# Performance work log

Measured on AMD Instinct MI355X. Metric: run time of the kernel, lower is better.

Reference implementation:

```python
import jax, jax.numpy as jnp
import numpy as np
from jax import lax

B, P, C = 2, 512, 5                 # images, proposals/img, classes (incl. background)
IN_FEAT, REP = 12544, 1024          # 256*7*7 pooled features; TwoMLPHead width
H_IMG = W_IMG = 800.0
SCORE_THRESH, NMS_THRESH, DET_PER_IMG = 0.05, 0.5, 100
MIN_SIZE = 0.01
WX, WY, WW, WH = 10.0, 10.0, 5.0, 5.0
BBOX_CLIP = float(np.log(1000.0 / 16.0))
NEG = -1e9


def _make_boxes(key, n):
    k1, k2, k3, k4 = jax.random.split(key, 4)
    cx = jax.random.uniform(k1, (n,)) * W_IMG
    cy = jax.random.uniform(k2, (n,)) * H_IMG
    bw = jax.random.uniform(k3, (n,)) * 180.0 + 20.0
    bh = jax.random.uniform(k4, (n,)) * 180.0 + 20.0
    x1 = jnp.clip(cx - bw / 2, 0.0, W_IMG)
    y1 = jnp.clip(cy - bh / 2, 0.0, H_IMG)
    x2 = jnp.clip(cx + bw / 2, 0.0, W_IMG)
    y2 = jnp.clip(cy + bh / 2, 0.0, H_IMG)
    return jnp.stack([x1, y1, x2, y2], -1).astype(jnp.float32)


def setup_inputs() -> dict:
    ks = jax.random.split(jax.random.key(0), 12)
    box_features = jax.random.normal(ks[0], (B * P, IN_FEAT), jnp.float32)
    proposals = jnp.stack([_make_boxes(ks[1 + i], P) for i in range(B)])
    def w(k, shp):
        return (jax.random.normal(k, shp, jnp.float32) / np.sqrt(shp[0])).astype(jnp.float32)
    return {
        'box_features': box_features,
        'proposals': proposals,
        'W1': w(ks[3], (IN_FEAT, REP)), 'b1': jnp.zeros((REP,), jnp.float32),
        'W2': w(ks[4], (REP, REP)),     'b2': jnp.zeros((REP,), jnp.float32),
        'Wc': w(ks[5], (REP, C)),       'bc': jnp.zeros((C,), jnp.float32),
        'Wb': w(ks[6], (REP, 4 * C)),   'bb': jnp.zeros((4 * C,), jnp.float32),
    }


def box_iou(a, b):
    area_a = (a[:, 2] - a[:, 0]) * (a[:, 3] - a[:, 1])
    area_b = (b[:, 2] - b[:, 0]) * (b[:, 3] - b[:, 1])
    lt = jnp.maximum(a[:, None, :2], b[None, :, :2])
    rb = jnp.minimum(a[:, None, 2:], b[None, :, 2:])
    wh = jnp.clip(rb - lt, 0.0)
    inter = wh[..., 0] * wh[..., 1]
    return inter / (area_a[:, None] + area_b[None, :] - inter + 1e-9)


def decode(reg, props):
    # reg: [N, C, 4] raw deltas; props: [N, 4] xyxy  (torchvision BoxCoder.decode)
    w = props[:, 2] - props[:, 0]
    h = props[:, 3] - props[:, 1]
    cx = props[:, 0] + 0.5 * w
    cy = props[:, 1] + 0.5 * h
    dx, dy = reg[..., 0] / WX, reg[..., 1] / WY
    dw = jnp.minimum(reg[..., 2] / WW, BBOX_CLIP)
    dh = jnp.minimum(reg[..., 3] / WH, BBOX_CLIP)
    pcx = dx * w[:, None] + cx[:, None]
    pcy = dy * h[:, None] + cy[:, None]
    pw = jnp.exp(dw) * w[:, None]
    ph = jnp.exp(dh) * h[:, None]
    return jnp.stack([pcx - 0.5 * pw, pcy - 0.5 * ph, pcx + 0.5 * pw, pcy + 0.5 * ph], -1)


def postprocess_one(boxes, scores, labels):
    # boxes [M,4] (already clipped), scores [M], labels [M] int; fixed-size output.
    M = boxes.shape[0]
    ws = boxes[:, 2] - boxes[:, 0]
    hs = boxes[:, 3] - boxes[:, 1]
    valid = (scores > SCORE_THRESH) & (ws >= MIN_SIZE) & (hs >= MIN_SIZE)
    order = jnp.argsort(-scores)
    b, s, l, v = boxes[order], scores[order], labels[order], valid[order]
    # batched (per-class) NMS via class-offset trick
    off = l.astype(b.dtype)[:, None] * (max(H_IMG, W_IMG) + 1.0)
    iou = box_iou(b + off, b + off)
    idxs = jnp.arange(M)

    def body(i, keep):
        sup = (iou[i] > NMS_THRESH) & keep[i] & (idxs > i)
        return keep & ~sup

    keep = lax.fori_loop(0, M, body, v)
    sc = jnp.where(keep, s, NEG)
    top_s, top_i = lax.top_k(sc, DET_PER_IMG)
    ok = top_s > NEG / 2
    tb = jnp.where(ok[:, None], b[top_i], 0.0)
    tl = jnp.where(ok, l[top_i], 0)
    ts = jnp.where(ok, top_s, 0.0)
    return tb, ts, tl


def reference(box_features, proposals, W1, b1, W2, b2, Wc, bc, Wb, bb):
    # box_head: TwoMLPHead
    h = jax.nn.relu(box_features @ W1 + b1)
    h = jax.nn.relu(h @ W2 + b2)
    # box_predictor
    class_logits = h @ Wc + bc                       # [N, C]
    box_regression = (h @ Wb + bb).reshape(-1, C, 4)  # [N, C, 4]
    props = proposals.reshape(-1, 4)
    pred = decode(box_regression, props)             # [N, C, 4]
    # clip to image
    pred = jnp.stack([
        jnp.clip(pred[..., 0], 0.0, W_IMG), jnp.clip(pred[..., 1], 0.0, H_IMG),
        jnp.clip(pred[..., 2], 0.0, W_IMG), jnp.clip(pred[..., 3], 0.0, H_IMG)], -1)
    scores = jax.nn.softmax(class_logits, -1)        # [N, C]
    # drop background class, flatten proposal-major (matches torch reshape(-1,4))
    pb = pred[:, 1:, :].reshape(B, P * (C - 1), 4)
    sc = scores[:, 1:].reshape(B, P * (C - 1))
    labels = jnp.tile(jnp.arange(1, C, dtype=jnp.int32), P)  # [M]
    boxes_o, scores_o, labels_o = jax.vmap(postprocess_one, in_axes=(0, 0, None))(pb, sc, labels)
    return boxes_o, scores_o, labels_o
```

## Files before the change

kernel.cpp:

```cpp
#include <hip/hip_runtime.h>
#include <math.h>

#define NROWS 1024
#define K1    12544
#define REP   1024
#define NDET  2048
#define DETS  100
#define BBOX_CLIP_F 4.135166556742356f

typedef __attribute__((ext_vector_type(8))) short bf16x8;
typedef __attribute__((ext_vector_type(4))) float f32x4;

__device__ __forceinline__ unsigned short rne_bf16(float x) {
  unsigned u = __float_as_uint(x);
  u += 0x7fffu + ((u >> 16) & 1u);
  return (unsigned short)(u >> 16);
}
__device__ __forceinline__ float bf16f(unsigned short h) {
  return __uint_as_float(((unsigned)h) << 16);
}
__device__ __forceinline__ int swz(int r, int s) {
  return s ^ (r & 3) ^ ((r >> 2) & 3);
}
__device__ __forceinline__ void gload16(const void* g, void* lds) {
  __builtin_amdgcn_global_load_lds(
      (const __attribute__((address_space(1))) unsigned int*)g,
      (__attribute__((address_space(3))) unsigned int*)lds, 16, 0, 0);
}

__global__ __launch_bounds__(256) void pack_b(
    const float* __restrict__ W, unsigned short* __restrict__ Oh,
    unsigned short* __restrict__ Ol, int nKB) {
  __shared__ unsigned short th[32 * 36], tl[32 * 36];
  const int kb = blockIdx.x, n0 = blockIdx.y * 32;
  const int t = threadIdx.x;
  const int r = t >> 3, c4 = (t & 7) << 2;
  float4 v = *(const float4*)&W[(size_t)(kb * 32 + r) * REP + n0 + c4];
  float fv[4] = {v.x, v.y, v.z, v.w};
#pragma unroll
  for (int j = 0; j < 4; ++j) {
    unsigned short h = rne_bf16(fv[j]);
    th[(c4 + j) * 36 + r] = h;
    tl[(c4 + j) * 36 + r] = rne_bf16(fv[j] - bf16f(h));
  }
  __syncthreads();
  const int half = t >> 7;
  const int n_loc = (t & 127) >> 2, slot = t & 3;
  const unsigned short* src = (half ? tl : th) + n_loc * 36 + slot * 8;
  ushort4 u0 = *(const ushort4*)src;
  ushort4 u1 = *(const ushort4*)(src + 4);
  const int n = n0 + n_loc, rb = n >> 7, rr = n & 127;
  size_t chunk = ((size_t)(rb * nKB + kb)) * 512 + rr * 4 + swz(rr, slot);
  unsigned short* dst = (half ? Ol : Oh) + chunk * 8;
  *(ushort4*)dst = u0;
  *(ushort4*)(dst + 4) = u1;
}

__global__ __launch_bounds__(256) void gemm_pk(
    const float* __restrict__ A, const unsigned short* __restrict__ Bh,
    const unsigned short* __restrict__ Bl, float* __restrict__ T,
    int K, int nKB, int stepsPerZ) {
  __shared__ __align__(16) unsigned short lds[2][4][4096];
  const int tid = threadIdx.x;
  const int w = tid >> 6, l = tid & 63;
  const int bm = blockIdx.x * 128;
  const int bnb = blockIdx.y;
  const int tk0 = blockIdx.z * stepsPerZ;
  const int arow = tid >> 1, ahalf = tid & 1;
  const int fr = l & 15, q = l >> 4;
  const int wr = (w >> 1) * 64, wc = (w & 1) * 64;
  const int qs = q ^ (fr & 3) ^ (fr >> 2);
  const int aoff = ((wr + fr) * 4 + qs) * 16;
  const int boff = ((wc + fr) * 4 + qs) * 16;
  const float* aptr = A + (size_t)(bm + arow) * K + ahalf * 16;

  float4 av[4];
  auto loadA = [&](int tk) {
    const float* p = aptr + tk * 32;
#pragma unroll
    for (int j = 0; j < 4; ++j) av[j] = *(const float4*)(p + j * 4);
  };
  auto stageB = [&](int bf, int tk) {
    const unsigned short* gh = Bh + ((size_t)(bnb * nKB + tk)) * 4096;
    const unsigned short* gl_ = Bl + ((size_t)(bnb * nKB + tk)) * 4096;
#pragma unroll
    for (int rseg = 0; rseg < 2; ++rseg) {
      const int seg = rseg * 4 + w;
      gload16(gh + (size_t)(seg * 64 + l) * 8, &lds[bf][2][seg * 512]);
      gload16(gl_ + (size_t)(seg * 64 + l) * 8, &lds[bf][3][seg * 512]);
    }
  };
  auto writeA = [&](int bf) {
#pragma unroll
    for (int j = 0; j < 2; ++j) {
      const int s_ = ahalf * 2 + j;
      float fv[8] = {av[j * 2].x, av[j * 2].y, av[j * 2].z, av[j * 2].w,
                     av[j * 2 + 1].x, av[j * 2 + 1].y, av[j * 2 + 1].z, av[j * 2 + 1].w};
      unsigned hp[4], lp[4];
#pragma unroll
      for (int p2 = 0; p2 < 4; ++p2) {
        unsigned short h0 = rne_bf16(fv[2 * p2]), h1 = rne_bf16(fv[2 * p2 + 1]);
        float l0 = fv[2 * p2] - bf16f(h0), l1 = fv[2 * p2 + 1] - bf16f(h1);
        hp[p2] = (unsigned)h0 | ((unsigned)h1 << 16);
        lp[p2] = (unsigned)rne_bf16(l0) | ((unsigned)rne_bf16(l1) << 16);
      }
      const int chunk = arow * 4 + swz(arow, s_);
      *(uint4*)&lds[bf][0][chunk * 8] = make_uint4(hp[0], hp[1], hp[2], hp[3]);
      *(uint4*)&lds[bf][1][chunk * 8] = make_uint4(lp[0], lp[1], lp[2], lp[3]);
    }
  };

  f32x4 acc[4][4];
#pragma unroll
  for (int m = 0; m < 4; ++m)
#pragma unroll
    for (int n = 0; n < 4; ++n) acc[m][n] = (f32x4){0.f, 0.f, 0.f, 0.f};

  loadA(tk0);
  stageB(0, tk0);
  writeA(0);
  __syncthreads();
  int cur = 0;
  for (int s = 0; s < stepsPerZ; ++s) {
    const bool nx = (s + 1 < stepsPerZ);
    if (nx) { loadA(tk0 + s + 1); stageB(cur ^ 1, tk0 + s + 1); }
    const char* La = (const char*)&lds[cur][0][0];
    const char* Ll = (const char*)&lds[cur][1][0];
    const char* Lbh = (const char*)&lds[cur][2][0];
    const char* Lbl = (const char*)&lds[cur][3][0];
    bf16x8 ah[4], al[4], bh[4], bl[4];
#pragma unroll
    for (int m = 0; m < 4; ++m) {
      ah[m] = *(const bf16x8*)(La + aoff + m * 1024);
      al[m] = *(const bf16x8*)(Ll + aoff + m * 1024);
    }
#pragma unroll
    for (int n = 0; n < 4; ++n) {
      bh[n] = *(const bf16x8*)(Lbh + boff + n * 1024);
      bl[n] = *(const bf16x8*)(Lbl + boff + n * 1024);
    }
#pragma unroll
    for (int m = 0; m < 4; ++m)
#pragma unroll
      for (int n = 0; n < 4; ++n) {
        acc[m][n] = __builtin_amdgcn_mfma_f32_16x16x32_bf16(ah[m], bh[n], acc[m][n], 0, 0, 0);
        acc[m][n] = __builtin_amdgcn_mfma_f32_16x16x32_bf16(ah[m], bl[n], acc[m][n], 0, 0, 0);
        acc[m][n] = __builtin_amdgcn_mfma_f32_16x16x32_bf16(al[m], bh[n], acc[m][n], 0, 0, 0);
      }
    if (nx) writeA(cur ^ 1);
    __syncthreads();
    cur ^= 1;
  }
  float* Tz = T + (size_t)blockIdx.z * (NROWS * REP);
#pragma unroll
  for (int m = 0; m < 4; ++m) {
    const int r0 = bm + wr + m * 16 + ((l >> 4) << 2);
#pragma unroll
    for (int n = 0; n < 4; ++n) {
      const int c = bnb * 128 + wc + n * 16 + fr;
#pragma unroll
      for (int j = 0; j < 4; ++j) Tz[(size_t)(r0 + j) * REP + c] = acc[m][n][j];
    }
  }
}

__global__ __launch_bounds__(256) void combine8_relu(
    const float* __restrict__ T, const float* __restrict__ bias, float* __restrict__ H) {
  const int i = blockIdx.x * 256 + threadIdx.x;
  const int MN4 = NROWS * REP / 4;
  const float4* t = (const float4*)T;
  float4 s0 = t[i];
#pragma unroll
  for (int z = 1; z < 8; ++z) {
    float4 v = t[i + z * MN4];
    s0.x += v.x; s0.y += v.y; s0.z += v.z; s0.w += v.w;
  }
  float4 bs = ((const float4*)bias)[i & 255];
  float4 r;
  r.x = fmaxf(s0.x + bs.x, 0.f);
  r.y = fmaxf(s0.y + bs.y, 0.f);
  r.z = fmaxf(s0.z + bs.z, 0.f);
  r.w = fmaxf(s0.w + bs.w, 0.f);
  ((float4*)H)[i] = r;
}

__global__ __launch_bounds__(256) void gemm64(
    const float* __restrict__ A, const float* __restrict__ W,
    float* __restrict__ T, int K, int N, int kChunk) {
  __shared__ float As[32][68];
  __shared__ float Bs[32][64];
  const int tid = threadIdx.x;
  const int bm = blockIdx.x * 64, bn = blockIdx.y * 64;
  const int k0 = blockIdx.z * kChunk;
  const int tx = tid & 15, ty = tid >> 4;
  const int ar = tid >> 3;
  const int ac = (tid & 7) << 2;
  const int br = tid >> 4;
  const int bc = (tid & 15) << 2;
  float acc[4][4] = {{0.f,0.f,0.f,0.f},{0.f,0.f,0.f,0.f},{0.f,0.f,0.f,0.f},{0.f,0.f,0.f,0.f}};
  for (int kk = k0; kk < k0 + kChunk; kk += 32) {
    float4 a0 = *(const float4*)&A[(size_t)(bm + ar) * K + kk + ac];
    float4 a1 = *(const float4*)&A[(size_t)(bm + ar + 32) * K + kk + ac];
    float4 b0 = *(const float4*)&W[(size_t)(kk + br) * N + bn + bc];
    float4 b1 = *(const float4*)&W[(size_t)(kk + br + 16) * N + bn + bc];
    As[ac+0][ar] = a0.x; As[ac+1][ar] = a0.y; As[ac+2][ar] = a0.z; As[ac+3][ar] = a0.w;
    As[ac+0][ar+32] = a1.x; As[ac+1][ar+32] = a1.y; As[ac+2][ar+32] = a1.z; As[ac+3][ar+32] = a1.w;
    *(float4*)&Bs[br][bc]    = b0;
    *(float4*)&Bs[br+16][bc] = b1;
    __syncthreads();
#pragma unroll
    for (int k = 0; k < 32; ++k) {
      float4 av = *(const float4*)&As[k][ty << 2];
      float4 bv = *(const float4*)&Bs[k][tx << 2];
      float a_[4] = {av.x, av.y, av.z, av.w};
      float b_[4] = {bv.x, bv.y, bv.z, bv.w};
#pragma unroll
      for (int i = 0; i < 4; ++i)
#pragma unroll
        for (int j = 0; j < 4; ++j)
          acc[i][j] = fmaf(a_[i], b_[j], acc[i][j]);
    }
    __syncthreads();
  }
  float* Tz = T + (size_t)blockIdx.z * NROWS * REP;
#pragma unroll
  for (int i = 0; i < 4; ++i) {
    float4 v = make_float4(acc[i][0], acc[i][1], acc[i][2], acc[i][3]);
    *(float4*)&Tz[(size_t)(bm + (ty << 2) + i) * N + bn + (tx << 2)] = v;
  }
}

__global__ __launch_bounds__(256) void combine_relu(
    const float* __restrict__ T, const float* __restrict__ bias, float* __restrict__ H) {
  const int i = blockIdx.x * 256 + threadIdx.x;
  const int MN4 = NROWS * REP / 4;
  const float4* t = (const float4*)T;
  float4 a = t[i], b = t[i + MN4], c = t[i + 2 * MN4], d = t[i + 3 * MN4];
  float4 bs = ((const float4*)bias)[i & 255];
  float4 r;
  r.x = fmaxf(((a.x + b.x) + (c.x + d.x)) + bs.x, 0.f);
  r.y = fmaxf(((a.y + b.y) + (c.y + d.y)) + bs.y, 0.f);
  r.z = fmaxf(((a.z + b.z) + (c.z + d.z)) + bs.z, 0.f);
  r.w = fmaxf(((a.w + b.w) + (c.w + d.w)) + bs.w, 0.f);
  ((float4*)H)[i] = r;
}

__global__ __launch_bounds__(256) void heads_kernel(
    const float* __restrict__ H2, const float* __restrict__ Wc, const float* __restrict__ bcv,
    const float* __restrict__ Wb, const float* __restrict__ bbv,
    const float* __restrict__ props, float* __restrict__ pb, float* __restrict__ sc) {
  const int n = blockIdx.x;
  __shared__ float hrow[REP];
  __shared__ float part[25][8];
  __shared__ float outv[25];
  __shared__ float smax[5];
  const int tid = threadIdx.x;
  ((float4*)hrow)[tid] = ((const float4*)(H2 + (size_t)n * REP))[tid];
  __syncthreads();
  if (tid < 200) {
    const int o = tid >> 3, s = tid & 7;
    float a = 0.f;
    if (o < 5) {
      const float* w = Wc + o;
      for (int k = s * 128; k < s * 128 + 128; ++k) a = fmaf(hrow[k], w[(size_t)k * 5], a);
    } else {
      const float* w = Wb + (o - 5);
      for (int k = s * 128; k < s * 128 + 128; ++k) a = fmaf(hrow[k], w[(size_t)k * 20], a);
    }
    part[o][s] = a;
  }
  __syncthreads();
  if (tid < 25) {
    float a = ((part[tid][0] + part[tid][1]) + (part[tid][2] + part[tid][3]))
            + ((part[tid][4] + part[tid][5]) + (part[tid][6] + part[tid][7]));
    a += (tid < 5) ? bcv[tid] : bbv[tid - 5];
    outv[tid] = a;
  }
  __syncthreads();
  if (tid == 0) {
    float m = outv[0];
    for (int c = 1; c < 5; ++c) m = fmaxf(m, outv[c]);
    float e[5], ssum = 0.f;
    for (int c = 0; c < 5; ++c) { e[c] = expf(outv[c] - m); ssum += e[c]; }
    for (int c = 0; c < 5; ++c) smax[c] = e[c] / ssum;
  }
  __syncthreads();
  if (tid < 4) {
    const int c = tid + 1;
    const float* pr = props + (size_t)n * 4;
    const float x1 = pr[0], y1 = pr[1], x2 = pr[2], y2 = pr[3];
    const float w = x2 - x1, h = y2 - y1;
    const float cx = x1 + 0.5f * w, cy = y1 + 0.5f * h;
    const float r0 = outv[5 + c * 4 + 0], r1 = outv[5 + c * 4 + 1];
    const float r2 = outv[5 + c * 4 + 2], r3 = outv[5 + c * 4 + 3];
    const float dx = r0 / 10.0f, dy = r1 / 10.0f;
    const float dw = fminf(r2 / 5.0f, BBOX_CLIP_F);
    const float dh = fminf(r3 / 5.0f, BBOX_CLIP_F);
    const float pcx = dx * w + cx, pcy = dy * h + cy;
    const float pw = expf(dw) * w, ph = expf(dh) * h;
    float bx1 = pcx - 0.5f * pw, by1 = pcy - 0.5f * ph;
    float bx2 = pcx + 0.5f * pw, by2 = pcy + 0.5f * ph;
    bx1 = fminf(fmaxf(bx1, 0.f), 800.f);
    by1 = fminf(fmaxf(by1, 0.f), 800.f);
    bx2 = fminf(fmaxf(bx2, 0.f), 800.f);
    by2 = fminf(fmaxf(by2, 0.f), 800.f);
    const int img = n >> 9;
    const int pidx = ((n & 511) << 2) + (c - 1);
    float* o = pb + (size_t)(img * NDET + pidx) * 4;
    o[0] = bx1; o[1] = by1; o[2] = bx2; o[3] = by2;
    sc[img * NDET + pidx] = smax[c];
  }
}

__global__ __launch_bounds__(1024) void sort_kernel(
    const float* __restrict__ sc, unsigned* __restrict__ sidx) {
  const int b = blockIdx.x;
  __shared__ unsigned long long key[NDET];
  const int tid = threadIdx.x;
  for (int t = tid; t < NDET; t += 1024) {
    unsigned bits = __float_as_uint(sc[b * NDET + t]);
    key[t] = ((unsigned long long)bits << 32) | (unsigned)(~t);
  }
  __syncthreads();
  for (int k = 2; k <= NDET; k <<= 1) {
    for (int j = k >> 1; j > 0; j >>= 1) {
      for (int t = tid; t < NDET; t += 1024) {
        const int ixj = t ^ j;
        if (ixj > t) {
          const bool up = (t & k) == 0;
          unsigned long long a = key[t], bb_ = key[ixj];
          if ((a < bb_) == up) { key[t] = bb_; key[ixj] = a; }
        }
      }
      __syncthreads();
    }
  }
  for (int t = tid; t < NDET; t += 1024)
    sidx[b * NDET + t] = ~(unsigned)key[t];
}

__global__ __launch_bounds__(256) void prep_kernel(
    const unsigned* __restrict__ sidx, const float* __restrict__ pb, const float* __restrict__ sc,
    float* __restrict__ sbox, float* __restrict__ soff, float* __restrict__ sscore,
    float* __restrict__ sarea, float* __restrict__ slab, unsigned* __restrict__ vword) {
  const int b = blockIdx.y;
  const int i = blockIdx.x * 256 + threadIdx.x;
  const unsigned oi = sidx[b * NDET + i];
  const float* bx = pb + (size_t)(b * NDET + oi) * 4;
  const float x1 = bx[0], y1 = bx[1], x2 = bx[2], y2 = bx[3];
  const float s = sc[b * NDET + oi];
  const float lab = (float)((oi & 3) + 1);
  const bool valid = (s > 0.05f) && ((x2 - x1) >= 0.01f) && ((y2 - y1) >= 0.01f);
  const float off = lab * 801.0f;
  float* sb = sbox + (size_t)(b * NDET + i) * 4;
  sb[0] = x1; sb[1] = y1; sb[2] = x2; sb[3] = y2;
  float* so = soff + (size_t)(b * NDET + i) * 4;
  so[0] = x1 + off; so[1] = y1 + off; so[2] = x2 + off; so[3] = y2 + off;
  sscore[b * NDET + i] = s;
  sarea[b * NDET + i] = (x2 - x1) * (y2 - y1);
  slab[b * NDET + i] = lab;
  const unsigned long long bal = __ballot(valid);
  if ((i & 31) == 0) vword[b * 64 + (i >> 5)] = (unsigned)(bal >> (i & 32));
}

__global__ __launch_bounds__(256) void mask_kernel(
    const float* __restrict__ soff, const float* __restrict__ sarea,
    unsigned* __restrict__ mask) {
  const int b = blockIdx.y;
  __shared__ float box[NDET][4];
  __shared__ float area[NDET];
  const int tid = threadIdx.x;
  const float4* src = (const float4*)(soff + (size_t)b * NDET * 4);
  for (int t = tid; t < NDET; t += 256) ((float4*)box)[t] = src[t];
  const float4* asrc = (const float4*)(sarea + (size_t)b * NDET);
  for (int t = tid; t < NDET / 4; t += 256) ((float4*)area)[t] = asrc[t];
  __syncthreads();
  const int li = tid >> 6;
  const int w  = tid & 63;
  const int i  = blockIdx.x * 4 + li;
  const float ax1 = box[i][0], ay1 = box[i][1], ax2 = box[i][2], ay2 = box[i][3];
  const float aa = area[i];
  unsigned bits = 0;
#pragma unroll 4
  for (int jj = 0; jj < 32; ++jj) {
    const int j = jj * 64 + w;
    const float ix = fmaxf(fminf(ax2, box[j][2]) - fmaxf(ax1, box[j][0]), 0.f);
    const float iy = fmaxf(fminf(ay2, box[j][3]) - fmaxf(ay1, box[j][1]), 0.f);
    const float inter = ix * iy;
    const float iou = inter / (aa + area[j] - inter + 1e-9f);
    if (j > i && iou > 0.5f) bits |= (1u << jj);
  }
  mask[((size_t)b * NDET + i) * 64 + w] = bits;
}

__global__ __launch_bounds__(64) void scan_kernel(
    const unsigned* __restrict__ vword, const unsigned* __restrict__ mask,
    const float* __restrict__ sbox, const float* __restrict__ sscore,
    const float* __restrict__ slab, float* __restrict__ out) {
  const int b = blockIdx.x;
  const int lane = threadIdx.x;
  const unsigned valid = vword[b * 64 + lane];
  unsigned sup = 0;
  __shared__ unsigned short klist[DETS];
  int kcnt = 0;
  for (int i = 0; i < NDET; ++i) {
    const unsigned v = __shfl(valid, i >> 5);
    if (!((v >> (i & 31)) & 1)) continue;
    const unsigned s = __shfl(sup, i & 63);
    if ((s >> (i >> 6)) & 1) continue;
    if (lane == 0) klist[kcnt] = (unsigned short)i;
    kcnt++;
    sup |= mask[((size_t)b * NDET + i) * 64 + lane];
    if (kcnt == DETS) break;
  }
  __syncthreads();
  for (int s = lane; s < DETS; s += 64) {
    float b0 = 0.f, b1 = 0.f, b2 = 0.f, b3 = 0.f, sv = 0.f, lv = 0.f;
    if (s < kcnt) {
      const int i = klist[s];
      const float* bx = sbox + ((size_t)b * NDET + i) * 4;
      b0 = bx[0]; b1 = bx[1]; b2 = bx[2]; b3 = bx[3];
      sv = sscore[b * NDET + i];
      lv = slab[b * NDET + i];
    }
    float* ob = out + ((size_t)b * DETS + s) * 4;
    ob[0] = b0; ob[1] = b1; ob[2] = b2; ob[3] = b3;
    out[2 * DETS * 4 + b * DETS + s] = sv;
    out[2 * DETS * 4 + 2 * DETS + b * DETS + s] = lv;
  }
}

extern "C" void kernel_launch(void* const* d_in, const int* in_sizes, int n_in,
                              void* d_out, int out_size, void* d_ws, size_t ws_size,
                              hipStream_t stream) {
  const float* X     = (const float*)d_in[0];
  const float* props = (const float*)d_in[1];
  const float* W1    = (const float*)d_in[2];
  const float* b1    = (const float*)d_in[3];
  const float* W2    = (const float*)d_in[4];
  const float* b2    = (const float*)d_in[5];
  const float* Wc    = (const float*)d_in[6];
  const float* bc    = (const float*)d_in[7];
  const float* Wb    = (const float*)d_in[8];
  const float* bb    = (const float*)d_in[9];
  float* out = (float*)d_out;

  const size_t NEED_MFMA =
      (size_t)(8 + 1 + 1) * 1048576 * 4 +
      (size_t)2 * (size_t)K1 * 1024 * 2 +
      (size_t)2 * 1048576 * 2 +
      (size_t)2500000;

  float *T, *H1, *H2, *pb, *sc;
  unsigned short *W1h = nullptr, *W1l = nullptr, *W2h = nullptr, *W2l = nullptr;
  const bool use_mfma = (ws_size >= NEED_MFMA);
  if (use_mfma) {
    T   = (float*)d_ws;
    H1  = T + 8 * 1048576;
    H2  = H1 + 1048576;
    W1h = (unsigned short*)(H2 + 1048576);
    W1l = W1h + (size_t)K1 * 1024;
    W2h = W1l + (size_t)K1 * 1024;
    W2l = W2h + 1048576;
    pb  = (float*)(W2l + 1048576);
  } else {
    T  = (float*)d_ws;
    H1 = T + 4 * 1048576;
    H2 = H1 + 1048576;
    pb = H2 + 1048576;
  }
  sc = pb + 2 * NDET * 4;
  unsigned* sidx = (unsigned*)(sc + 2 * NDET);
  float* sbox   = (float*)(sidx + 2 * NDET);
  float* soff   = sbox + 2 * NDET * 4;
  float* sscore = soff + 2 * NDET * 4;
  float* sarea  = sscore + 2 * NDET;
  float* slab   = sarea + 2 * NDET;
  unsigned* vword = (unsigned*)(slab + 2 * NDET);
  unsigned* mask  = vword + 128;

  if (use_mfma) {
    pack_b<<<dim3(K1 / 32, 32), 256, 0, stream>>>(W1, W1h, W1l, K1 / 32);
    pack_b<<<dim3(32, 32), 256, 0, stream>>>(W2, W2h, W2l, 32);
    gemm_pk<<<dim3(8, 8, 8), 256, 0, stream>>>(X, W1h, W1l, T, K1, K1 / 32, 49);
    combine8_relu<<<1024, 256, 0, stream>>>(T, b1, H1);
    gemm_pk<<<dim3(8, 8, 8), 256, 0, stream>>>(H1, W2h, W2l, T, REP, 32, 4);
    combine8_relu<<<1024, 256, 0, stream>>>(T, b2, H2);
  } else {
    gemm64<<<dim3(16, 16, 4), 256, 0, stream>>>(X, W1, T, K1, REP, K1 / 4);
    combine_relu<<<1024, 256, 0, stream>>>(T, b1, H1);
    gemm64<<<dim3(16, 16, 4), 256, 0, stream>>>(H1, W2, T, REP, REP, REP / 4);
    combine_relu<<<1024, 256, 0, stream>>>(T, b2, H2);
  }
  heads_kernel<<<1024, 256, 0, stream>>>(H2, Wc, bc, Wb, bb, props, pb, sc);
  sort_kernel<<<2, 1024, 0, stream>>>(sc, sidx);
  prep_kernel<<<dim3(8, 2), 256, 0, stream>>>(sidx, pb, sc, sbox, soff, sscore, sarea, slab, vword);
  mask_kernel<<<dim3(512, 2), 256, 0, stream>>>(soff, sarea, mask);
  scan_kernel<<<2, 64, 0, stream>>>(vword, mask, sbox, sscore, slab, out);
}
```

Measured before the change: 267.5 us.

## Pre-pack activations into split bf16 swizzled layout for both MLP GEMMs

Adds a pack_a kernel that converts the input features once into hi/lo bf16 tiles in the swizzled chunk layout, and a gemm_pk2 kernel that stages A and B tiles from global memory with direct 16-byte loads instead of converting A in the main loop. The first layer's combine step now writes H1 straight into the packed hi/lo format for the second GEMM. The aim is to take fp32-to-bf16 conversion and register staging out of the GEMM inner loop. In exchange it needs a larger workspace (a new path gated on ws_size) and an extra full pass over the 50 MB input.

```diff
diff --git a/kernel.cpp b/kernel.cpp
--- a/kernel.cpp
+++ b/kernel.cpp
@@ -54,6 +54,180 @@
   unsigned short* dst = (half ? Ol : Oh) + chunk * 8;
   *(ushort4*)dst = u0;
   *(ushort4*)(dst + 4) = u1;
+}
+
+__global__ __launch_bounds__(256) void pack_a(
+    const float* __restrict__ A, unsigned short* __restrict__ Oh,
+    unsigned short* __restrict__ Ol, int K, int nKB) {
+  const int kb = blockIdx.x;
+  const int r = blockIdx.y * 64 + (threadIdx.x >> 2);
+  const int slot = threadIdx.x & 3;
+  const float* p = A + (size_t)r * K + kb * 32 + slot * 8;
+  float4 f0 = *(const float4*)p;
+  float4 f1 = *(const float4*)(p + 4);
+  float fv[8] = {f0.x, f0.y, f0.z, f0.w, f1.x, f1.y, f1.z, f1.w};
+  ushort4 uh0, uh1, ul0, ul1;
+  unsigned short hh[8], ll[8];
+#pragma unroll
+  for (int j = 0; j < 8; ++j) {
+    hh[j] = rne_bf16(fv[j]);
+    ll[j] = rne_bf16(fv[j] - bf16f(hh[j]));
+  }
+  uh0 = make_ushort4(hh[0], hh[1], hh[2], hh[3]);
+  uh1 = make_ushort4(hh[4], hh[5], hh[6], hh[7]);
+  ul0 = make_ushort4(ll[0], ll[1], ll[2], ll[3]);
+  ul1 = make_ushort4(ll[4], ll[5], ll[6], ll[7]);
+  const int rb = r >> 7, rr = r & 127;
+  size_t chunk = ((size_t)(rb * nKB + kb)) * 512 + rr * 4 + swz(rr, slot);
+  unsigned short* dh = Oh + chunk * 8;
+  unsigned short* dl = Ol + chunk * 8;
+  *(ushort4*)dh = uh0; *(ushort4*)(dh + 4) = uh1;
+  *(ushort4*)dl = ul0; *(ushort4*)(dl + 4) = ul1;
+}
+
+__global__ __launch_bounds__(256) void gemm_pk2(
+    const unsigned short* __restrict__ Ah, const unsigned short* __restrict__ Al,
+    const unsigned short* __restrict__ Bh, const unsigned short* __restrict__ Bl,
+    float* __restrict__ T, int nKB, int stepsPerZ) {
+  __shared__ __align__(16) unsigned short lds[2][4][4096];
+  const int tid = threadIdx.x;
+  const int w = tid >> 6, l = tid & 63;
+  const int rbA = blockIdx.x, rbB = blockIdx.y;
+  const int tk0 = blockIdx.z * stepsPerZ;
+  const int fr = l & 15, q = l >> 4;
+  const int wr = (w >> 1) * 64, wc = (w & 1) * 64;
+  const int qs = q ^ (fr & 3) ^ (fr >> 2);
+  const int aoff = ((wr + fr) * 4 + qs) * 16;
+  const int boff = ((wc + fr) * 4 + qs) * 16;
+
+  auto stage = [&](int bf, int tk) {
+    const unsigned short* ga_h = Ah + ((size_t)(rbA * nKB + tk)) * 4096;
+    const unsigned short* ga_l = Al + ((size_t)(rbA * nKB + tk)) * 4096;
+    const unsigned short* gb_h = Bh + ((size_t)(rbB * nKB + tk)) * 4096;
+    const unsigned short* gb_l = Bl + ((size_t)(rbB * nKB + tk)) * 4096;
+#pragma unroll
+    for (int rseg = 0; rseg < 2; ++rseg) {
+      const int seg = rseg * 4 + w;
+      const size_t go = (size_t)(seg * 64 + l) * 8;
+      gload16(ga_h + go, &lds[bf][0][seg * 512]);
+      gload16(ga_l + go, &lds[bf][1][seg * 512]);
+      gload16(gb_h + go, &lds[bf][2][seg * 512]);
+      gload16(gb_l + go, &lds[bf][3][seg * 512]);
+    }
+  };
+
+  f32x4 acc[4][4];
+#pragma unroll
+  for (int m = 0; m < 4; ++m)
+#pragma unroll
+    for (int n = 0; n < 4; ++n) acc[m][n] = (f32x4){0.f, 0.f, 0.f, 0.f};
+
+  stage(0, tk0);
+  __syncthreads();
+  int cur = 0;
+  for (int s = 0; s < stepsPerZ; ++s) {
+    if (s + 1 < stepsPerZ) stage(cur ^ 1, tk0 + s + 1);
+    const char* La  = (const char*)&lds[cur][0][0];
+    const char* Ll  = (const char*)&lds[cur][1][0];
+    const char* Lbh = (const char*)&lds[cur][2][0];
+    const char* Lbl = (const char*)&lds[cur][3][0];
+    bf16x8 ah[4], al[4], bh[4], bl[4];
+#pragma unroll
+    for (int m = 0; m < 4; ++m) {
+      ah[m] = *(const bf16x8*)(La + aoff + m * 1024);
+      al[m] = *(const bf16x8*)(Ll + aoff + m * 1024);
+    }
+#pragma unroll
+    for (int n = 0; n < 4; ++n) {
+      bh[n] = *(const bf16x8*)(Lbh + boff + n * 1024);
+      bl[n] = *(const bf16x8*)(Lbl + boff + n * 1024);
+    }
+#pragma unroll
+    for (int m = 0; m < 4; ++m)
+#pragma unroll
+      for (int n = 0; n < 4; ++n) {
+        acc[m][n] = __builtin_amdgcn_mfma_f32_16x16x32_bf16(ah[m], bh[n], acc[m][n], 0, 0, 0);
+        acc[m][n] = __builtin_amdgcn_mfma_f32_16x16x32_bf16(ah[m], bl[n], acc[m][n], 0, 0, 0);
+        acc[m][n] = __builtin_amdgcn_mfma_f32_16x16x32_bf16(al[m], bh[n], acc[m][n], 0, 0, 0);
+      }
+    __syncthreads();
+    cur ^= 1;
+  }
+  float* Tz = T + (size_t)blockIdx.z * (NROWS * REP);
+#pragma unroll
+  for (int m = 0; m < 4; ++m) {
+    const int r0 = rbA * 128 + wr + m * 16 + ((l >> 4) << 2);
+#pragma unroll
+    for (int n = 0; n < 4; ++n) {
+      const int c = rbB * 128 + wc + n * 16 + fr;
+#pragma unroll
+      for (int j = 0; j < 4; ++j) Tz[(size_t)(r0 + j) * REP + c] = acc[m][n][j];
+    }
+  }
+}
+
+__global__ __launch_bounds__(256) void combine8_relu_pack(
+    const float* __restrict__ T, const float* __restrict__ bias,
+    unsigned short* __restrict__ Oh, unsigned short* __restrict__ Ol) {
+  const int e = (blockIdx.x * 256 + threadIdx.x) * 8;
+  const int MN = NROWS * REP;
+  float s[8];
+  {
+    float4 a0 = *(const float4*)&T[e];
+    float4 a1 = *(const float4*)&T[e + 4];
+    s[0] = a0.x; s[1] = a0.y; s[2] = a0.z; s[3] = a0.w;
+    s[4] = a1.x; s[5] = a1.y; s[6] = a1.z; s[7] = a1.w;
+  }
+#pragma unroll
+  for (int z = 1; z < 8; ++z) {
+    float4 a0 = *(const float4*)&T[z * MN + e];
+    float4 a1 = *(const float4*)&T[z * MN + e + 4];
+    s[0] += a0.x; s[1] += a0.y; s[2] += a0.z; s[3] += a0.w;
+    s[4] += a1.x; s[5] += a1.y; s[6] += a1.z; s[7] += a1.w;
+  }
+  const int c0 = e & 1023;
+  float4 b0 = *(const float4*)&bias[c0];
+  float4 b1 = *(const float4*)&bias[c0 + 4];
+  s[0] = fmaxf(s[0] + b0.x, 0.f); s[1] = fmaxf(s[1] + b0.y, 0.f);
+  s[2] = fmaxf(s[2] + b0.z, 0.f); s[3] = fmaxf(s[3] + b0.w, 0.f);
+  s[4] = fmaxf(s[4] + b1.x, 0.f); s[5] = fmaxf(s[5] + b1.y, 0.f);
+  s[6] = fmaxf(s[6] + b1.z, 0.f); s[7] = fmaxf(s[7] + b1.w, 0.f);
+  unsigned short hh[8], ll[8];
+#pragma unroll
+  for (int j = 0; j < 8; ++j) {
+    hh[j] = rne_bf16(s[j]);
+    ll[j] = rne_bf16(s[j] - bf16f(hh[j]));
+  }
+  const int r = e >> 10;
+  const int kb = c0 >> 5, slot = (c0 >> 3) & 3;
+  const int rb = r >> 7, rr = r & 127;
+  size_t chunk = ((size_t)(rb * 32 + kb)) * 512 + rr * 4 + swz(rr, slot);
+  unsigned short* dh = Oh + chunk * 8;
+  unsigned short* dl = Ol + chunk * 8;
+  *(ushort4*)dh = make_ushort4(hh[0], hh[1], hh[2], hh[3]);
+  *(ushort4*)(dh + 4) = make_ushort4(hh[4], hh[5], hh[6], hh[7]);
+  *(ushort4*)dl = make_ushort4(ll[0], ll[1], ll[2], ll[3]);
+  *(ushort4*)(dl + 4) = make_ushort4(ll[4], ll[5], ll[6], ll[7]);
+}
+
+__global__ __launch_bounds__(256) void combine8_relu(
+    const float* __restrict__ T, const float* __restrict__ bias, float* __restrict__ H) {
+  const int i = blockIdx.x * 256 + threadIdx.x;
+  const int MN4 = NROWS * REP / 4;
+  const float4* t = (const float4*)T;
+  float4 s0 = t[i];
+#pragma unroll
+  for (int z = 1; z < 8; ++z) {
+    float4 v = t[i + z * MN4];
+    s0.x += v.x; s0.y += v.y; s0.z += v.z; s0.w += v.w;
+  }
+  float4 bs = ((const float4*)bias)[i & 255];
+  float4 r;
+  r.x = fmaxf(s0.x + bs.x, 0.f);
+  r.y = fmaxf(s0.y + bs.y, 0.f);
+  r.z = fmaxf(s0.z + bs.z, 0.f);
+  r.w = fmaxf(s0.w + bs.w, 0.f);
+  ((float4*)H)[i] = r;
 }
 
 __global__ __launch_bounds__(256) void gemm_pk(
@@ -162,26 +336,6 @@
       for (int j = 0; j < 4; ++j) Tz[(size_t)(r0 + j) * REP + c] = acc[m][n][j];
     }
   }
-}
-
-__global__ __launch_bounds__(256) void combine8_relu(
-    const float* __restrict__ T, const float* __restrict__ bias, float* __restrict__ H) {
-  const int i = blockIdx.x * 256 + threadIdx.x;
-  const int MN4 = NROWS * REP / 4;
-  const float4* t = (const float4*)T;
-  float4 s0 = t[i];
-#pragma unroll
-  for (int z = 1; z < 8; ++z) {
-    float4 v = t[i + z * MN4];
-    s0.x += v.x; s0.y += v.y; s0.z += v.z; s0.w += v.w;
-  }
-  float4 bs = ((const float4*)bias)[i & 255];
-  float4 r;
-  r.x = fmaxf(s0.x + bs.x, 0.f);
-  r.y = fmaxf(s0.y + bs.y, 0.f);
-  r.z = fmaxf(s0.z + bs.z, 0.f);
-  r.w = fmaxf(s0.w + bs.w, 0.f);
-  ((float4*)H)[i] = r;
 }
 
 __global__ __launch_bounds__(256) void gemm64(
@@ -445,16 +599,33 @@
   const float* bb    = (const float*)d_in[9];
   float* out = (float*)d_out;
 
-  const size_t NEED_MFMA =
-      (size_t)(8 + 1 + 1) * 1048576 * 4 +
+  const size_t POST_B = 3000000;
+  const size_t NEED_BIG =
+      (size_t)9 * 1048576 * 4 +
+      (size_t)4 * (size_t)K1 * 1024 * 2 +
+      (size_t)4 * 1048576 * 2 + POST_B;
+  const size_t NEED_MID =
+      (size_t)10 * 1048576 * 4 +
       (size_t)2 * (size_t)K1 * 1024 * 2 +
-      (size_t)2 * 1048576 * 2 +
-      (size_t)2500000;
-
-  float *T, *H1, *H2, *pb, *sc;
+      (size_t)2 * 1048576 * 2 + 2500000;
+
+  float *T, *H1 = nullptr, *H2, *pb, *sc;
   unsigned short *W1h = nullptr, *W1l = nullptr, *W2h = nullptr, *W2l = nullptr;
-  const bool use_mfma = (ws_size >= NEED_MFMA);
-  if (use_mfma) {
+  unsigned short *Ahp = nullptr, *Alp = nullptr, *H1h = nullptr, *H1l = nullptr;
+  const int path = (ws_size >= NEED_BIG) ? 2 : (ws_size >= NEED_MID) ? 1 : 0;
+  if (path == 2) {
+    T   = (float*)d_ws;
+    H2  = T + 8 * 1048576;
+    W1h = (unsigned short*)(H2 + 1048576);
+    W1l = W1h + (size_t)K1 * 1024;
+    W2h = W1l + (size_t)K1 * 1024;
+    W2l = W2h + 1048576;
+    Ahp = W2l + 1048576;
+    Alp = Ahp + (size_t)K1 * 1024;
+    H1h = Alp + (size_t)K1 * 1024;
+    H1l = H1h + 1048576;
+    pb  = (float*)(H1l + 1048576);
+  } else if (path == 1) {
     T   = (float*)d_ws;
     H1  = T + 8 * 1048576;
     H2  = H1 + 1048576;
@@ -479,7 +650,15 @@
   unsigned* vword = (unsigned*)(slab + 2 * NDET);
   unsigned* mask  = vword + 128;
 
-  if (use_mfma) {
+  if (path == 2) {
+    pack_b<<<dim3(K1 / 32, 32), 256, 0, stream>>>(W1, W1h, W1l, K1 / 32);
+    pack_b<<<dim3(32, 32), 256, 0, stream>>>(W2, W2h, W2l, 32);
+    pack_a<<<dim3(K1 / 32, 16), 256, 0, stream>>>(X, Ahp, Alp, K1, K1 / 32);
+    gemm_pk2<<<dim3(8, 8, 8), 256, 0, stream>>>(Ahp, Alp, W1h, W1l, T, K1 / 32, 49);
+    combine8_relu_pack<<<512, 256, 0, stream>>>(T, b1, H1h, H1l);
+    gemm_pk2<<<dim3(8, 8, 8), 256, 0, stream>>>(H1h, H1l, W2h, W2l, T, 32, 4);
+    combine8_relu<<<1024, 256, 0, stream>>>(T, b2, H2);
+  } else if (path == 1) {
     pack_b<<<dim3(K1 / 32, 32), 256, 0, stream>>>(W1, W1h, W1l, K1 / 32);
     pack_b<<<dim3(32, 32), 256, 0, stream>>>(W2, W2h, W2l, 32);
     gemm_pk<<<dim3(8, 8, 8), 256, 0, stream>>>(X, W1h, W1l, T, K1, K1 / 32, 49);
```

After: 253.5 us. 1.06x faster.
